# Optimization experiments

Hardware: AMD Instinct MI355X
Metric: run time of the kernel (lower is better)

## Reference

```python
import jax, jax.numpy as jnp
import numpy as np

B, H, W, C = 64, 28, 28, 384
NH, WS = 12, 7
KD = C // NH            # key_dim = head_dim = 32 (attn_ratio=1.0 -> d = KD)
QKV_OUT = 3 * KD * NH   # 1152
HID = 4 * C             # mlp hidden
N = WS * WS             # tokens per window
L = H * W
SCALE = KD ** -0.5
EPS_LN = 1e-5
EPS_BN = 1e-5


def _make_bias_idxs():
    pts = [(i, j) for i in range(WS) for j in range(WS)]
    offs, idxs = {}, []
    for p1 in pts:
        for p2 in pts:
            o = (abs(p1[0] - p2[0]), abs(p1[1] - p2[1]))
            if o not in offs:
                offs[o] = len(offs)
            idxs.append(offs[o])
    return np.asarray(idxs, dtype=np.int32).reshape(N, N)


def _ln(x, g, b):
    m = jnp.mean(x, axis=-1, keepdims=True)
    v = jnp.mean(jnp.square(x - m), axis=-1, keepdims=True)
    return (x - m) * jax.lax.rsqrt(v + EPS_LN) * g + b


def setup_inputs() -> dict:
    key = jax.random.key(0)
    ks = jax.random.split(key, 8)
    s = 0.02
    return {
        "x": jax.random.normal(ks[0], (B, L, C), jnp.float32),
        "ln_a_g": jnp.ones((C,), jnp.float32),
        "ln_a_b": jnp.zeros((C,), jnp.float32),
        "qkv_w": jax.random.normal(ks[1], (QKV_OUT, C), jnp.float32) * s,
        "qkv_b": jnp.zeros((QKV_OUT,), jnp.float32),
        "attn_bias": jax.random.normal(ks[2], (NH, N), jnp.float32) * s,
        "proj_w": jax.random.normal(ks[3], (C, C), jnp.float32) * s,
        "proj_b": jnp.zeros((C,), jnp.float32),
        "conv_w": jax.random.normal(ks[4], (C, 1, 3, 3), jnp.float32) * s,
        "bn_g": jnp.ones((C,), jnp.float32),
        "bn_b": jnp.zeros((C,), jnp.float32),
        "bn_m": jnp.zeros((C,), jnp.float32),
        "bn_v": jnp.ones((C,), jnp.float32),
        "ln_m_g": jnp.ones((C,), jnp.float32),
        "ln_m_b": jnp.zeros((C,), jnp.float32),
        "fc1_w": jax.random.normal(ks[5], (HID, C), jnp.float32) * s,
        "fc1_b": jnp.zeros((HID,), jnp.float32),
        "fc2_w": jax.random.normal(ks[6], (C, HID), jnp.float32) * s,
        "fc2_b": jnp.zeros((C,), jnp.float32),
        "bias_idxs": jnp.asarray(_make_bias_idxs()),
    }


def reference(x, ln_a_g, ln_a_b, qkv_w, qkv_b, attn_bias, proj_w, proj_b,
              conv_w, bn_g, bn_b, bn_m, bn_v, ln_m_g, ln_m_b,
              fc1_w, fc1_b, fc2_w, fc2_b, bias_idxs):
    res = x
    nh, nw = H // WS, W // WS
    # window partition: [B,L,C] -> [B*nWin, N, C]
    xw = x.reshape(B, nh, WS, nw, WS, C).transpose(0, 1, 3, 2, 4, 5)
    xw = xw.reshape(B * nh * nw, N, C)
    # attention
    xn = _ln(xw, ln_a_g, ln_a_b)
    qkv = xn @ qkv_w.T + qkv_b                       # [Bw, N, 3*NH*KD]
    qkv = qkv.reshape(-1, N, NH, 3 * KD).transpose(0, 2, 1, 3)
    q, k, v = qkv[..., :KD], qkv[..., KD:2 * KD], qkv[..., 2 * KD:]
    bias = attn_bias[:, bias_idxs]                   # [NH, N, N]
    attn = jnp.einsum('bhnd,bhmd->bhnm', q, k) * SCALE + bias
    attn = jax.nn.softmax(attn, axis=-1)
    o = jnp.einsum('bhnm,bhmd->bhnd', attn, v)
    o = o.transpose(0, 2, 1, 3).reshape(-1, N, C)
    o = o @ proj_w.T + proj_b
    # window unpartition -> [B, L, C]
    o = o.reshape(B, nh, nw, WS, WS, C).transpose(0, 1, 3, 2, 4, 5).reshape(B, L, C)
    x = res + o
    # depthwise ConvBN (inference BN)
    xc = x.transpose(0, 2, 1).reshape(B, C, H, W)
    xc = jax.lax.conv_general_dilated(
        xc, conv_w, (1, 1), 'SAME', feature_group_count=C,
        dimension_numbers=('NCHW', 'OIHW', 'NCHW'))
    inv = jax.lax.rsqrt(bn_v + EPS_BN)
    xc = (xc - bn_m[None, :, None, None]) * (bn_g * inv)[None, :, None, None] + bn_b[None, :, None, None]
    x = xc.reshape(B, C, L).transpose(0, 2, 1)
    # MLP residual
    h = _ln(x, ln_m_g, ln_m_b)
    h = jax.nn.gelu(h @ fc1_w.T + fc1_b, approximate=False)
    h = h @ fc2_w.T + fc2_b
    return x + h
```

## Files before the change

### kernel.cpp

```cpp
#include <hip/hip_runtime.h>
#include <hip/hip_bf16.h>
#include <stdint.h>

#define BATCH 64
#define CC 384
#define NHEAD 12
#define KD 32
#define NTOK 49
#define LL 784
#define MTOT 50176
#define HID 1536
#define QKV_OUT 1152
#define SCALE 0.17677669529663687f
#define EPS 1e-5f

typedef __bf16 bf16x8 __attribute__((ext_vector_type(8)));
typedef float f32x4 __attribute__((ext_vector_type(4)));

__device__ __forceinline__ float bf2f(unsigned short u) {
  union { unsigned int u; float f; } cv; cv.u = ((unsigned int)u) << 16; return cv.f;
}
__device__ __forceinline__ unsigned short f2bf(float f) {
  union { float f; unsigned int u; } cv; cv.f = f;
  unsigned int r = cv.u + 0x7FFFu + ((cv.u >> 16) & 1u);
  return (unsigned short)(r >> 16);
}
__device__ __forceinline__ void gl_lds16(const unsigned short* g, unsigned short* l) {
  __builtin_amdgcn_global_load_lds(
      (const __attribute__((address_space(1))) unsigned int*)g,
      (__attribute__((address_space(3))) unsigned int*)l, 16, 0, 0);
}
__device__ __forceinline__ int winrow(int m) {
  int wi = m / 49, nn = m - wi * 49;
  int bb = wi >> 4, wb = wi & 15;
  int hs = nn / 7, wsx = nn - hs * 7;
  return bb * LL + (wb >> 2) * 196 + hs * 28 + (wb & 3) * 7 + wsx;
}

__global__ void detect_kernel(const unsigned short* __restrict__ x, int* flag) {
  __shared__ int cnt;
  if (threadIdx.x == 0) cnt = 0;
  __syncthreads();
  int c = 0;
  for (int i = threadIdx.x; i < 4096; i += 256) {
    if (((x[i] >> 7) & 0xFF) == 0xFF) c++;
  }
  atomicAdd(&cnt, c);
  __syncthreads();
  if (threadIdx.x == 0) *flag = (cnt > 0) ? 1 : 0;
}

struct CvtArgs {
  const void* src[19];
  unsigned int n[19];
  unsigned int off[19];
};
__global__ __launch_bounds__(256) void convert_kernel(
    CvtArgs a, unsigned short* __restrict__ dst, const int* __restrict__ flag) {
  const int which = blockIdx.y;
  const unsigned int nn = a.n[which];
  unsigned short* d = dst + a.off[which];
  const unsigned int stride = gridDim.x * blockDim.x;
  const unsigned int idx = blockIdx.x * blockDim.x + threadIdx.x;
  const unsigned int ng = nn >> 3;
  if (*flag) {
    const float* s = (const float*)a.src[which];
    for (unsigned int g = idx; g < ng; g += stride) {
      const float4 f0 = ((const float4*)s)[g * 2];
      const float4 f1 = ((const float4*)s)[g * 2 + 1];
      ushort4 lo, hi;
      lo.x = f2bf(f0.x); lo.y = f2bf(f0.y); lo.z = f2bf(f0.z); lo.w = f2bf(f0.w);
      hi.x = f2bf(f1.x); hi.y = f2bf(f1.y); hi.z = f2bf(f1.z); hi.w = f2bf(f1.w);
      ((ushort4*)d)[g * 2] = lo;
      ((ushort4*)d)[g * 2 + 1] = hi;
    }
    for (unsigned int i = ng * 8 + idx; i < nn; i += stride) d[i] = f2bf(s[i]);
  } else {
    const unsigned short* s = (const unsigned short*)a.src[which];
    for (unsigned int g = idx; g < ng; g += stride)
      ((uint4*)d)[g] = ((const uint4*)s)[g];
    for (unsigned int i = ng * 8 + idx; i < nn; i += stride) d[i] = s[i];
  }
}

__global__ __launch_bounds__(256) void bias_kernel(
    const unsigned short* __restrict__ cAb, const int* __restrict__ bias_idxs,
    float* __restrict__ bias_full) {
  const int h = blockIdx.x;
  for (int i = threadIdx.x; i < NTOK * NTOK; i += 256)
    bias_full[h * NTOK * NTOK + i] = bf2f(cAb[h * NTOK + bias_idxs[i]]);
}

__global__ __launch_bounds__(384) void prep_kernel(
    const unsigned short* __restrict__ cw, const unsigned short* __restrict__ bg,
    const unsigned short* __restrict__ bb, const unsigned short* __restrict__ bm,
    const unsigned short* __restrict__ bv,
    unsigned short* __restrict__ cwT, float* __restrict__ bnsc, float* __restrict__ bnsh) {
  const int c = threadIdx.x;
  const float sc = bf2f(bg[c]) * rsqrtf(bf2f(bv[c]) + EPS);
  bnsc[c] = sc;
  bnsh[c] = bf2f(bb[c]) - bf2f(bm[c]) * sc;
  #pragma unroll
  for (int t = 0; t < 9; ++t) cwT[t * CC + c] = cw[c * 9 + t];
}

__global__ __launch_bounds__(384) void fold_kernel(
    const unsigned short* __restrict__ W, const unsigned short* __restrict__ g,
    const unsigned short* __restrict__ bvec, const unsigned short* __restrict__ b2,
    unsigned short* __restrict__ W2, float* __restrict__ S, float* __restrict__ C) {
  const int n = blockIdx.x, k = threadIdx.x;
  const float w = bf2f(W[(size_t)n * CC + k]);
  const float gw = bf2f(g[k]) * w;
  const unsigned short r = f2bf(gw);
  W2[(size_t)n * CC + k] = r;
  float s = bf2f(r);
  float c = bf2f(bvec[k]) * w;
  #pragma unroll
  for (int off = 32; off; off >>= 1) { s += __shfl_xor(s, off); c += __shfl_xor(c, off); }
  __shared__ float s6[6], c6[6];
  const int wv = k >> 6;
  if ((k & 63) == 0) { s6[wv] = s; c6[wv] = c; }
  __syncthreads();
  if (k == 0) {
    float st = 0.f, ct = 0.f;
    #pragma unroll
    for (int i = 0; i < 6; ++i) { st += s6[i]; ct += c6[i]; }
    S[n] = st; C[n] = ct + bf2f(b2[n]);
  }
}

__global__ __launch_bounds__(128) void statsA_kernel(
    const unsigned short* __restrict__ x, float* __restrict__ muA, float* __restrict__ invA) {
  const int tid = threadIdx.x;
  const int wi = blockIdx.y, n = blockIdx.x;
  const int l = (((wi & 15) >> 2) * 196 + (n / 7) * 28 + (wi & 3) * 7 + (n % 7));
  const unsigned short* xr = x + ((size_t)(wi >> 4) * LL + l) * CC;
  float s = 0.f, sq = 0.f;
  #pragma unroll
  for (int j = 0; j < 3; ++j) {
    const float v = bf2f(xr[tid + 128 * j]);
    s += v; sq += v * v;
  }
  #pragma unroll
  for (int off = 32; off; off >>= 1) { s += __shfl_xor(s, off); sq += __shfl_xor(sq, off); }
  __shared__ float red[4];
  const int wv = tid >> 6;
  if ((tid & 63) == 0) { red[wv] = s; red[2 + wv] = sq; }
  __syncthreads();
  if (tid == 0) {
    const float tot = red[0] + red[1], totq = red[2] + red[3];
    const float mean = tot * (1.f / CC);
    const float var = totq * (1.f / CC) - mean * mean;
    muA[(size_t)wi * NTOK + n] = mean;
    invA[(size_t)wi * NTOK + n] = rsqrtf(var + EPS);
  }
}

enum { EP_PLAIN = 0, EP_WINRES = 2, EP_RES2 = 3, EP_QKV = 4, EP_GELU2 = 5 };

template <int EP>
__global__ __launch_bounds__(256) void gemm128(
    const unsigned short* __restrict__ A, const unsigned short* __restrict__ W,
    const unsigned short* __restrict__ bias, const unsigned short* __restrict__ res,
    void* __restrict__ outp, int K, int N, int m_off, const int* __restrict__ flagp,
    int Nt, const float* __restrict__ muv, const float* __restrict__ invv,
    const float* __restrict__ snv, const float* __restrict__ cnv) {
  constexpr bool GATHER = (EP == EP_QKV);
  constexpr bool LNFOLD = (EP == EP_QKV || EP == EP_GELU2);
  __shared__ __align__(16) unsigned short lds[3 * 8192];
  const int tid = threadIdx.x;
  const int lane = tid & 63;
  const int wave = tid >> 6;
  const int nwg = gridDim.x;
  const int id = blockIdx.x;
  const int q8 = nwg >> 3, r8 = nwg & 7;
  const int xcd = id & 7, rank = id >> 3;
  const int wgid = (xcd < r8 ? xcd * (q8 + 1) : r8 * (q8 + 1) + (xcd - r8) * q8) + rank;
  const int bm = (wgid / Nt) * 128;
  const int bn = (wgid - (wgid / Nt) * Nt) * 128;
  const int wm = (wave >> 1) * 64;
  const int wn = (wave & 1) * 64;
  const int srow = tid >> 2;
  const int sr15 = srow & 15;
  const int sp = (sr15 + (sr15 >> 2)) & 3;
  const int s_col = ((tid & 3) ^ sp) * 8;
  int rowA0, rowA1;
  if (GATHER) {
    rowA0 = winrow(bm + srow + m_off);
    rowA1 = winrow(bm + srow + 64 + m_off);
  } else {
    rowA0 = bm + srow; rowA1 = rowA0 + 64;
  }
  const unsigned short* ApA = A + (size_t)rowA0 * K + s_col;
  const unsigned short* ApB = A + (size_t)rowA1 * K + s_col;
  const unsigned short* Wp0 = W + (size_t)(bn + srow) * K + s_col;
  const size_t rstep = (size_t)64 * K;
  f32x4 acc[4][4] = {};
  const int fr = lane & 15;
  const int quad = lane >> 4;
  const int nt = K >> 5;
  const int rp = (fr + (fr >> 2)) & 3;
  const int cg = (quad ^ rp) * 8;

  auto stage = [&](int bsel, int t) {
    unsigned short* al = lds + bsel * 8192 + tid * 8;
    unsigned short* bl = al + 4096;
    gl_lds16(ApA + t * 32, al);
    gl_lds16(ApB + t * 32, al + 2048);
    gl_lds16(Wp0 + t * 32, bl);
    gl_lds16(Wp0 + t * 32 + rstep, bl + 2048);
  };

  stage(0, 0);
  stage(1, 1);
  int b = 0;
  for (int t = 0; t < nt; ++t) {
    if (t + 1 < nt) asm volatile("s_waitcnt vmcnt(4)" ::: "memory");
    else            asm volatile("s_waitcnt vmcnt(0)" ::: "memory");
    __builtin_amdgcn_s_barrier();
    __builtin_amdgcn_sched_barrier(0);
    if (t + 2 < nt) stage(b ? b - 1 : 2, t + 2);
    const unsigned short* Ab = lds + b * 8192;
    const unsigned short* Bb = Ab + 4096;
    bf16x8 af[4], bfr[4];
    #pragma unroll
    for (int i = 0; i < 4; ++i) {
      af[i]  = *(const bf16x8*)(Ab + (wm + i * 16 + fr) * 32 + cg);
      bfr[i] = *(const bf16x8*)(Bb + (wn + i * 16 + fr) * 32 + cg);
    }
    #pragma unroll
    for (int i = 0; i < 4; ++i)
      #pragma unroll
      for (int j = 0; j < 4; ++j)
        acc[i][j] = __builtin_amdgcn_mfma_f32_16x16x32_bf16(af[i], bfr[j], acc[i][j], 0, 0, 0);
    asm volatile("s_waitcnt lgkmcnt(0)" ::: "memory");
    __builtin_amdgcn_sched_barrier(0);
    b = (b == 2) ? 0 : b + 1;
  }

  int isf32 = 0;
  if (EP == EP_RES2) isf32 = *flagp;
  const int qr = quad * 4;
  float s4[4], c4[4], bvs[4];
  #pragma unroll
  for (int tj = 0; tj < 4; ++tj) {
    const int n = bn + wn + tj * 16 + fr;
    if (LNFOLD) { s4[tj] = snv[n]; c4[tj] = cnv[n]; }
    else        { bvs[tj] = bf2f(bias[n]); }
  }
  #pragma unroll
  for (int ti = 0; ti < 4; ++ti) {
    #pragma unroll
    for (int r = 0; r < 4; ++r) {
      const int mr = bm + wm + ti * 16 + qr + r;
      float iv = 0.f, um = 0.f;
      if (LNFOLD) { iv = invv[mr + m_off]; um = muv[mr + m_off] * iv; }
      size_t rowbase;
      if (EP == EP_WINRES)      rowbase = (size_t)winrow(mr) * CC;
      else if (EP == EP_RES2)   rowbase = (size_t)(mr + m_off) * N;
      else                      rowbase = (size_t)mr * N;
      #pragma unroll
      for (int tj = 0; tj < 4; ++tj) {
        const int n = bn + wn + tj * 16 + fr;
        if (EP == EP_QKV) {
          const float v = iv * acc[ti][tj][r] - um * s4[tj] + c4[tj];
          ((unsigned short*)outp)[rowbase + n] = f2bf(v);
        } else if (EP == EP_GELU2) {
          float v = iv * acc[ti][tj][r] - um * s4[tj] + c4[tj];
          const float t2 = v * (1.5957691216f + 0.0713548162f * v * v);
          v = __fdividef(v, 1.0f + __expf(-t2));
          ((unsigned short*)outp)[rowbase + n] = f2bf(v);
        } else if (EP == EP_WINRES) {
          const size_t idx = rowbase + n;
          float v = acc[ti][tj][r] + bvs[tj] + bf2f(res[idx]);
          ((unsigned short*)outp)[idx] = f2bf(v);
        } else if (EP == EP_RES2) {
          const size_t idx = rowbase + n;
          float v = acc[ti][tj][r] + bvs[tj] + bf2f(res[idx]);
          if (isf32) ((float*)outp)[idx] = v;
          else       ((unsigned short*)outp)[idx] = f2bf(v);
        } else {
          ((unsigned short*)outp)[rowbase + n] = f2bf(acc[ti][tj][r] + bvs[tj]);
        }
      }
    }
  }
}

__global__ __launch_bounds__(64) void attn_mfma(
    const unsigned short* __restrict__ qkv, const float* __restrict__ bias_full,
    unsigned short* __restrict__ o, int wi_off) {
  __shared__ __align__(16) unsigned short Pl[64 * 72];
  __shared__ __align__(16) unsigned short vT[32 * 72];
  const int wi = blockIdx.x, h = blockIdx.y;
  const int lane = threadIdx.x;
  const int l15 = lane & 15;
  const int quad = lane >> 4;
  const unsigned short* base = qkv + (size_t)wi * NTOK * QKV_OUT + h * 96;

  bf16x8 qf[4], kf[4];
  #pragma unroll
  for (int i = 0; i < 4; ++i) {
    const int n = i * 16 + l15;
    if (n < NTOK) {
      const unsigned short* p = base + (size_t)n * QKV_OUT + quad * 8;
      qf[i] = *(const bf16x8*)(p);
      kf[i] = *(const bf16x8*)(p + 32);
    } else {
      qf[i] = (bf16x8)0; kf[i] = (bf16x8)0;
    }
  }

  for (int idx = lane; idx < 32 * 72; idx += 64) vT[idx] = 0;
  __syncthreads();
  for (int idx = lane; idx < NTOK * KD; idx += 64) {
    const int m = idx >> 5, d = idx & 31;
    vT[d * 72 + m] = base[(size_t)m * QKV_OUT + 64 + d];
  }

  f32x4 acc[4][4] = {};
  #pragma unroll
  for (int i = 0; i < 4; ++i)
    #pragma unroll
    for (int j = 0; j < 4; ++j)
      acc[i][j] = __builtin_amdgcn_mfma_f32_16x16x32_bf16(qf[i], kf[j], acc[i][j], 0, 0, 0);

  const float* bh = bias_full + h * NTOK * NTOK;
  float rinv[4][4];
  #pragma unroll
  for (int i = 0; i < 4; ++i) {
    #pragma unroll
    for (int r = 0; r < 4; ++r) {
      const int n = i * 16 + quad * 4 + r;
      float sv[4];
      #pragma unroll
      for (int j = 0; j < 4; ++j) {
        const int m = j * 16 + l15;
        float s = acc[i][j][r] * SCALE;
        if (n < NTOK && m < NTOK) s += bh[n * NTOK + m];
        if (m >= NTOK) s = -1e30f;
        sv[j] = s;
      }
      float mx = fmaxf(fmaxf(sv[0], sv[1]), fmaxf(sv[2], sv[3]));
      #pragma unroll
      for (int t = 1; t < 16; t <<= 1) mx = fmaxf(mx, __shfl_xor(mx, t));
      float sum = 0.f;
      #pragma unroll
      for (int j = 0; j < 4; ++j) {
        const float p = __expf(sv[j] - mx);
        sum += p;
        Pl[n * 72 + j * 16 + l15] = f2bf(p);
      }
      #pragma unroll
      for (int t = 1; t < 16; t <<= 1) sum += __shfl_xor(sum, t);
      rinv[i][r] = 1.f / sum;
    }
  }
  __syncthreads();

  f32x4 acc2[4][2] = {};
  #pragma unroll
  for (int kk = 0; kk < 2; ++kk) {
    bf16x8 pf[4], vf[2];
    #pragma unroll
    for (int i = 0; i < 4; ++i)
      pf[i] = *(const bf16x8*)(Pl + (i * 16 + l15) * 72 + kk * 32 + quad * 8);
    #pragma unroll
    for (int jd = 0; jd < 2; ++jd)
      vf[jd] = *(const bf16x8*)(vT + (jd * 16 + l15) * 72 + kk * 32 + quad * 8);
    #pragma unroll
    for (int i = 0; i < 4; ++i)
      #pragma unroll
      for (int jd = 0; jd < 2; ++jd)
        acc2[i][jd] = __builtin_amdgcn_mfma_f32_16x16x32_bf16(pf[i], vf[jd], acc2[i][jd], 0, 0, 0);
  }

  #pragma unroll
  for (int i = 0; i < 4; ++i) {
    #pragma unroll
    for (int r = 0; r < 4; ++r) {
      const int n = i * 16 + quad * 4 + r;
      if (n < NTOK) {
        const float ri = rinv[i][r];
        #pragma unroll
        for (int jd = 0; jd < 2; ++jd) {
          const int d = jd * 16 + l15;
          o[((size_t)(wi_off + wi) * NTOK + n) * CC + h * KD + d] = f2bf(acc2[i][jd][r] * ri);
        }
      }
    }
  }
}

__global__ __launch_bounds__(384) void conv_bn_ln(
    const unsigned short* __restrict__ x1, const unsigned short* __restrict__ cwT,
    const float* __restrict__ bnsc, const float* __restrict__ bnsh,
    unsigned short* __restrict__ x2, float* __restrict__ muM, float* __restrict__ invM) {
  __shared__ float rs[8][48], rq[8][48];
  const int tid = threadIdx.x;
  const int pos = tid / 48;
  const int c8 = tid - pos * 48;
  const int c0 = c8 * 8;
  const int hw = blockIdx.x * 8 + pos;
  const int b = blockIdx.y;
  const int h = hw / 28, w = hw - h * 28;
  float acc[8] = {};
  #pragma unroll
  for (int t = 0; t < 9; ++t) {
    const int dh = t / 3 - 1, dw = t % 3 - 1;
    const int hh = h + dh, ww = w + dw;
    if (hh >= 0 && hh < 28 && ww >= 0 && ww < 28) {
      const uint4 xv = *(const uint4*)(x1 + ((size_t)b * LL + hh * 28 + ww) * CC + c0);
      const uint4 wv = *(const uint4*)(cwT + t * CC + c0);
      const unsigned short* xp = (const unsigned short*)&xv;
      const unsigned short* wp = (const unsigned short*)&wv;
      #pragma unroll
      for (int k = 0; k < 8; ++k) acc[k] += bf2f(xp[k]) * bf2f(wp[k]);
    }
  }
  const float4 sc0 = *(const float4*)(bnsc + c0);
  const float4 sc1 = *(const float4*)(bnsc + c0 + 4);
  const float4 sh0 = *(const float4*)(bnsh + c0);
  const float4 sh1 = *(const float4*)(bnsh + c0 + 4);
  float y[8];
  y[0] = acc[0] * sc0.x + sh0.x; y[1] = acc[1] * sc0.y + sh0.y;
  y[2] = acc[2] * sc0.z + sh0.z; y[3] = acc[3] * sc0.w + sh0.w;
  y[4] = acc[4] * sc1.x + sh1.x; y[5] = acc[5] * sc1.y + sh1.y;
  y[6] = acc[6] * sc1.z + sh1.z; y[7] = acc[7] * sc1.w + sh1.w;
  unsigned short yr[8];
  #pragma unroll
  for (int k = 0; k < 8; ++k) yr[k] = f2bf(y[k]);
  ushort4 pk0, pk1;
  pk0.x = yr[0]; pk0.y = yr[1]; pk0.z = yr[2]; pk0.w = yr[3];
  pk1.x = yr[4]; pk1.y = yr[5]; pk1.z = yr[6]; pk1.w = yr[7];
  const size_t row = ((size_t)b * LL + hw) * CC + c0;
  *(ushort4*)(x2 + row) = pk0;
  *(ushort4*)(x2 + row + 4) = pk1;
  float s = 0.f, q = 0.f;
  #pragma unroll
  for (int k = 0; k < 8; ++k) { const float v = bf2f(yr[k]); s += v; q += v * v; }
  rs[pos][c8] = s; rq[pos][c8] = q;
  __syncthreads();
  if (c8 == 0) {
    float tot = 0.f, tq = 0.f;
    #pragma unroll 8
    for (int i = 0; i < 48; ++i) { tot += rs[pos][i]; tq += rq[pos][i]; }
    const float mean = tot * (1.f / CC);
    const float var = tq * (1.f / CC) - mean * mean;
    muM[(size_t)b * LL + hw] = mean;
    invM[(size_t)b * LL + hw] = rsqrtf(var + EPS);
  }
}

extern "C" void kernel_launch(void* const* d_in, const int* in_sizes, int n_in,
                              void* d_out, int out_size, void* d_ws, size_t ws_size,
                              hipStream_t stream) {
  int* flag = (int*)d_ws;
  unsigned short* base = (unsigned short*)d_ws;

  CvtArgs args;
  size_t cur = 32;
  size_t off[19];
  for (int i = 0; i < 19; ++i) {
    off[i] = cur;
    args.src[i] = d_in[i];
    args.n[i] = (unsigned int)in_sizes[i];
    args.off[i] = (unsigned int)cur;
    cur += ((size_t)in_sizes[i] + 63) & ~(size_t)63;
  }
  const unsigned short* cx   = base + off[0];
  const unsigned short* cgA  = base + off[1];
  const unsigned short* cbA  = base + off[2];
  const unsigned short* cQw  = base + off[3];
  const unsigned short* cQb  = base + off[4];
  const unsigned short* cAb  = base + off[5];
  const unsigned short* cPw  = base + off[6];
  const unsigned short* cPb  = base + off[7];
  const unsigned short* cCw  = base + off[8];
  const unsigned short* cBg  = base + off[9];
  const unsigned short* cBb  = base + off[10];
  const unsigned short* cBm  = base + off[11];
  const unsigned short* cBv  = base + off[12];
  const unsigned short* cMg  = base + off[13];
  const unsigned short* cMb  = base + off[14];
  const unsigned short* cF1w = base + off[15];
  const unsigned short* cF1b = base + off[16];
  const unsigned short* cF2w = base + off[17];
  const unsigned short* cF2b = base + off[18];
  const int* bias_idxs = (const int*)d_in[19];

  const size_t SZ = (size_t)MTOT * CC;
  const size_t tbl_bytes = 4 * (size_t)MTOT * 4 +
                           ((size_t)QKV_OUT + HID) * CC * 2 +
                           2 * ((size_t)QKV_OUT + HID) * 4 + 65536;
  const size_t need_full_bytes =
      (cur + SZ + (size_t)MTOT * HID) * 2 + tbl_bytes + 1024 * 1024;
  const int nchunk = (ws_size >= need_full_bytes) ? 1 : 2;
  const int MC = MTOT / nchunk;
  const int WC = 1024 / nchunk;
  const size_t buf2_cap = (size_t)MC * HID;

  unsigned short* o_buf = base + cur;
  unsigned short* buf2  = o_buf + SZ;
  unsigned short* x2    = base + off[0];
  float* bias_full = (float*)(buf2 + buf2_cap);
  unsigned short* cwT = (unsigned short*)(bias_full + 12 * NTOK * NTOK);
  float* bnsc = (float*)(cwT + 9 * CC);
  float* bnsh = bnsc + CC;
  float* muA  = bnsh + CC;
  float* invA = muA + MTOT;
  float* muM  = invA + MTOT;
  float* invM = muM + MTOT;
  float* sq   = invM + MTOT;
  float* cq   = sq + QKV_OUT;
  float* sm   = cq + QKV_OUT;
  float* cm   = sm + HID;
  unsigned short* W2q = (unsigned short*)(cm + HID);
  unsigned short* W2m = W2q + (size_t)QKV_OUT * CC;

  detect_kernel<<<1, 256, 0, stream>>>((const unsigned short*)d_in[0], flag);
  convert_kernel<<<dim3(512, 19), 256, 0, stream>>>(args, base, flag);
  bias_kernel<<<NHEAD, 256, 0, stream>>>(cAb, bias_idxs, bias_full);
  prep_kernel<<<1, 384, 0, stream>>>(cCw, cBg, cBb, cBm, cBv, cwT, bnsc, bnsh);
  fold_kernel<<<QKV_OUT, 384, 0, stream>>>(cQw, cgA, cbA, cQb, W2q, sq, cq);
  fold_kernel<<<HID, 384, 0, stream>>>(cF1w, cMg, cMb, cF1b, W2m, sm, cm);

  statsA_kernel<<<dim3(49, 1024), 128, 0, stream>>>(cx, muA, invA);

  for (int c = 0; c < nchunk; ++c) {
    gemm128<EP_QKV><<<(MC / 128) * (QKV_OUT / 128), 256, 0, stream>>>(
        cx, W2q, nullptr, nullptr, buf2, CC, QKV_OUT, c * MC, nullptr,
        QKV_OUT / 128, muA, invA, sq, cq);
    attn_mfma<<<dim3(WC, NHEAD), 64, 0, stream>>>(buf2, bias_full, o_buf, c * WC);
  }

  gemm128<EP_WINRES><<<(MTOT / 128) * (CC / 128), 256, 0, stream>>>(
      o_buf, cPw, cPb, cx, d_out, CC, CC, 0, nullptr, CC / 128,
      nullptr, nullptr, nullptr, nullptr);

  conv_bn_ln<<<dim3(98, BATCH), 384, 0, stream>>>(
      (const unsigned short*)d_out, cwT, bnsc, bnsh, x2, muM, invM);

  for (int c = 0; c < nchunk; ++c) {
    gemm128<EP_GELU2><<<(MC / 128) * (HID / 128), 256, 0, stream>>>(
        x2 + (size_t)c * MC * CC, W2m, nullptr, nullptr, buf2, CC, HID, c * MC,
        nullptr, HID / 128, muM, invM, sm, cm);
    gemm128<EP_RES2><<<(MC / 128) * (CC / 128), 256, 0, stream>>>(
        buf2, cF2w, cF2b, x2, d_out, HID, CC, c * MC, flag, CC / 128,
        nullptr, nullptr, nullptr, nullptr);
  }
}
```

Measured before the change: 679.5 us.

## Move window gather out of GEMMs into attention kernel indexing

The QKV GEMM and the projection GEMM now work on rows in flat image order, so they load and store contiguously without the per-row winrow gather and scatter. The attention kernel does the window partition itself, computing flat row indices for each token when it reads qkv and writes its output. LayerNorm mean and inverse std are packed into a float2 so the epilogue does one load per row. This removes address math and scattered accesses from the GEMMs, at the cost of strided window accesses inside the attention kernel. With two chunks the window-to-row mapping must stay aligned with the chunk boundary, which it does because 512 windows times 49 rows equals 25088.

```diff
diff --git a/kernel.cpp b/kernel.cpp
--- a/kernel.cpp
+++ b/kernel.cpp
@@ -29,12 +29,6 @@
   __builtin_amdgcn_global_load_lds(
       (const __attribute__((address_space(1))) unsigned int*)g,
       (__attribute__((address_space(3))) unsigned int*)l, 16, 0, 0);
-}
-__device__ __forceinline__ int winrow(int m) {
-  int wi = m / 49, nn = m - wi * 49;
-  int bb = wi >> 4, wb = wi & 15;
-  int hs = nn / 7, wsx = nn - hs * 7;
-  return bb * LL + (wb >> 2) * 196 + hs * 28 + (wb & 3) * 7 + wsx;
 }
 
 __global__ void detect_kernel(const unsigned short* __restrict__ x, int* flag) {
@@ -130,11 +124,10 @@
 }
 
 __global__ __launch_bounds__(128) void statsA_kernel(
-    const unsigned short* __restrict__ x, float* __restrict__ muA, float* __restrict__ invA) {
+    const unsigned short* __restrict__ x, float2* __restrict__ mui) {
   const int tid = threadIdx.x;
-  const int wi = blockIdx.y, n = blockIdx.x;
-  const int l = (((wi & 15) >> 2) * 196 + (n / 7) * 28 + (wi & 3) * 7 + (n % 7));
-  const unsigned short* xr = x + ((size_t)(wi >> 4) * LL + l) * CC;
+  const size_t row = (size_t)blockIdx.y * LL + blockIdx.x;
+  const unsigned short* xr = x + row * CC;
   float s = 0.f, sq = 0.f;
   #pragma unroll
   for (int j = 0; j < 3; ++j) {
@@ -151,22 +144,20 @@
     const float tot = red[0] + red[1], totq = red[2] + red[3];
     const float mean = tot * (1.f / CC);
     const float var = totq * (1.f / CC) - mean * mean;
-    muA[(size_t)wi * NTOK + n] = mean;
-    invA[(size_t)wi * NTOK + n] = rsqrtf(var + EPS);
-  }
-}
-
-enum { EP_PLAIN = 0, EP_WINRES = 2, EP_RES2 = 3, EP_QKV = 4, EP_GELU2 = 5 };
+    mui[row] = make_float2(mean, rsqrtf(var + EPS));
+  }
+}
+
+enum { EP_RES = 2, EP_RES2 = 3, EP_LNF = 4, EP_GELU2 = 5 };
 
 template <int EP>
 __global__ __launch_bounds__(256) void gemm128(
     const unsigned short* __restrict__ A, const unsigned short* __restrict__ W,
     const unsigned short* __restrict__ bias, const unsigned short* __restrict__ res,
     void* __restrict__ outp, int K, int N, int m_off, const int* __restrict__ flagp,
-    int Nt, const float* __restrict__ muv, const float* __restrict__ invv,
+    int Nt, const float2* __restrict__ mui,
     const float* __restrict__ snv, const float* __restrict__ cnv) {
-  constexpr bool GATHER = (EP == EP_QKV);
-  constexpr bool LNFOLD = (EP == EP_QKV || EP == EP_GELU2);
+  constexpr bool LNFOLD = (EP == EP_LNF || EP == EP_GELU2);
   __shared__ __align__(16) unsigned short lds[3 * 8192];
   const int tid = threadIdx.x;
   const int lane = tid & 63;
@@ -184,15 +175,7 @@
   const int sr15 = srow & 15;
   const int sp = (sr15 + (sr15 >> 2)) & 3;
   const int s_col = ((tid & 3) ^ sp) * 8;
-  int rowA0, rowA1;
-  if (GATHER) {
-    rowA0 = winrow(bm + srow + m_off);
-    rowA1 = winrow(bm + srow + 64 + m_off);
-  } else {
-    rowA0 = bm + srow; rowA1 = rowA0 + 64;
-  }
-  const unsigned short* ApA = A + (size_t)rowA0 * K + s_col;
-  const unsigned short* ApB = A + (size_t)rowA1 * K + s_col;
+  const unsigned short* Ap0 = A + (size_t)(bm + srow) * K + s_col;
   const unsigned short* Wp0 = W + (size_t)(bn + srow) * K + s_col;
   const size_t rstep = (size_t)64 * K;
   f32x4 acc[4][4] = {};
@@ -205,8 +188,8 @@
   auto stage = [&](int bsel, int t) {
     unsigned short* al = lds + bsel * 8192 + tid * 8;
     unsigned short* bl = al + 4096;
-    gl_lds16(ApA + t * 32, al);
-    gl_lds16(ApB + t * 32, al + 2048);
+    gl_lds16(Ap0 + t * 32, al);
+    gl_lds16(Ap0 + t * 32 + rstep, al + 2048);
     gl_lds16(Wp0 + t * 32, bl);
     gl_lds16(Wp0 + t * 32 + rstep, bl + 2048);
   };
@@ -254,15 +237,15 @@
     for (int r = 0; r < 4; ++r) {
       const int mr = bm + wm + ti * 16 + qr + r;
       float iv = 0.f, um = 0.f;
-      if (LNFOLD) { iv = invv[mr + m_off]; um = muv[mr + m_off] * iv; }
-      size_t rowbase;
-      if (EP == EP_WINRES)      rowbase = (size_t)winrow(mr) * CC;
-      else if (EP == EP_RES2)   rowbase = (size_t)(mr + m_off) * N;
-      else                      rowbase = (size_t)mr * N;
+      if (LNFOLD) {
+        const float2 mi = mui[mr + m_off];
+        iv = mi.y; um = mi.x * mi.y;
+      }
+      const size_t rowbase = (size_t)mr * N;
       #pragma unroll
       for (int tj = 0; tj < 4; ++tj) {
         const int n = bn + wn + tj * 16 + fr;
-        if (EP == EP_QKV) {
+        if (EP == EP_LNF) {
           const float v = iv * acc[ti][tj][r] - um * s4[tj] + c4[tj];
           ((unsigned short*)outp)[rowbase + n] = f2bf(v);
         } else if (EP == EP_GELU2) {
@@ -270,17 +253,15 @@
           const float t2 = v * (1.5957691216f + 0.0713548162f * v * v);
           v = __fdividef(v, 1.0f + __expf(-t2));
           ((unsigned short*)outp)[rowbase + n] = f2bf(v);
-        } else if (EP == EP_WINRES) {
+        } else if (EP == EP_RES) {
           const size_t idx = rowbase + n;
-          float v = acc[ti][tj][r] + bvs[tj] + bf2f(res[idx]);
+          const float v = acc[ti][tj][r] + bvs[tj] + bf2f(res[idx]);
           ((unsigned short*)outp)[idx] = f2bf(v);
-        } else if (EP == EP_RES2) {
+        } else {
           const size_t idx = rowbase + n;
-          float v = acc[ti][tj][r] + bvs[tj] + bf2f(res[idx]);
+          const float v = acc[ti][tj][r] + bvs[tj] + bf2f(res[idx]);
           if (isf32) ((float*)outp)[idx] = v;
           else       ((unsigned short*)outp)[idx] = f2bf(v);
-        } else {
-          ((unsigned short*)outp)[rowbase + n] = f2bf(acc[ti][tj][r] + bvs[tj]);
         }
       }
     }
@@ -289,21 +270,27 @@
 
 __global__ __launch_bounds__(64) void attn_mfma(
     const unsigned short* __restrict__ qkv, const float* __restrict__ bias_full,
-    unsigned short* __restrict__ o, int wi_off) {
+    unsigned short* __restrict__ o, int wi_off, int row_off) {
   __shared__ __align__(16) unsigned short Pl[64 * 72];
   __shared__ __align__(16) unsigned short vT[32 * 72];
-  const int wi = blockIdx.x, h = blockIdx.y;
+  const int wi = wi_off + blockIdx.x, h = blockIdx.y;
   const int lane = threadIdx.x;
   const int l15 = lane & 15;
   const int quad = lane >> 4;
-  const unsigned short* base = qkv + (size_t)wi * NTOK * QKV_OUT + h * 96;
+  const int bb = wi >> 4, wb = wi & 15;
+  const int wrow0 = bb * LL + (wb >> 2) * 196 + (wb & 3) * 7;
+  auto flatrow = [&](int n) {
+    const int h7 = n / 7;
+    return wrow0 + h7 * 28 + (n - h7 * 7);
+  };
 
   bf16x8 qf[4], kf[4];
   #pragma unroll
   for (int i = 0; i < 4; ++i) {
     const int n = i * 16 + l15;
     if (n < NTOK) {
-      const unsigned short* p = base + (size_t)n * QKV_OUT + quad * 8;
+      const unsigned short* p =
+          qkv + (size_t)(flatrow(n) - row_off) * QKV_OUT + h * 96 + quad * 8;
       qf[i] = *(const bf16x8*)(p);
       kf[i] = *(const bf16x8*)(p + 32);
     } else {
@@ -315,7 +302,7 @@
   __syncthreads();
   for (int idx = lane; idx < NTOK * KD; idx += 64) {
     const int m = idx >> 5, d = idx & 31;
-    vT[d * 72 + m] = base[(size_t)m * QKV_OUT + 64 + d];
+    vT[d * 72 + m] = qkv[(size_t)(flatrow(m) - row_off) * QKV_OUT + h * 96 + 64 + d];
   }
 
   f32x4 acc[4][4] = {};
@@ -382,10 +369,11 @@
       const int n = i * 16 + quad * 4 + r;
       if (n < NTOK) {
         const float ri = rinv[i][r];
+        const size_t orow = (size_t)flatrow(n) * CC + h * KD;
         #pragma unroll
         for (int jd = 0; jd < 2; ++jd) {
           const int d = jd * 16 + l15;
-          o[((size_t)(wi_off + wi) * NTOK + n) * CC + h * KD + d] = f2bf(acc2[i][jd][r] * ri);
+          o[orow + d] = f2bf(acc2[i][jd][r] * ri);
         }
       }
     }
@@ -395,7 +383,7 @@
 __global__ __launch_bounds__(384) void conv_bn_ln(
     const unsigned short* __restrict__ x1, const unsigned short* __restrict__ cwT,
     const float* __restrict__ bnsc, const float* __restrict__ bnsh,
-    unsigned short* __restrict__ x2, float* __restrict__ muM, float* __restrict__ invM) {
+    unsigned short* __restrict__ x2, float2* __restrict__ mui) {
   __shared__ float rs[8][48], rq[8][48];
   const int tid = threadIdx.x;
   const int pos = tid / 48;
@@ -447,8 +435,7 @@
     for (int i = 0; i < 48; ++i) { tot += rs[pos][i]; tq += rq[pos][i]; }
     const float mean = tot * (1.f / CC);
     const float var = tq * (1.f / CC) - mean * mean;
-    muM[(size_t)b * LL + hw] = mean;
-    invM[(size_t)b * LL + hw] = rsqrtf(var + EPS);
+    mui[(size_t)b * LL + hw] = make_float2(mean, rsqrtf(var + EPS));
   }
 }
 
@@ -490,7 +477,7 @@
   const int* bias_idxs = (const int*)d_in[19];
 
   const size_t SZ = (size_t)MTOT * CC;
-  const size_t tbl_bytes = 4 * (size_t)MTOT * 4 +
+  const size_t tbl_bytes = 2 * (size_t)MTOT * 8 +
                            ((size_t)QKV_OUT + HID) * CC * 2 +
                            2 * ((size_t)QKV_OUT + HID) * 4 + 65536;
   const size_t need_full_bytes =
@@ -507,11 +494,9 @@
   unsigned short* cwT = (unsigned short*)(bias_full + 12 * NTOK * NTOK);
   float* bnsc = (float*)(cwT + 9 * CC);
   float* bnsh = bnsc + CC;
-  float* muA  = bnsh + CC;
-  float* invA = muA + MTOT;
-  float* muM  = invA + MTOT;
-  float* invM = muM + MTOT;
-  float* sq   = invM + MTOT;
+  float2* muiA = (float2*)(bnsh + CC);
+  float2* muiM = muiA + MTOT;
+  float* sq   = (float*)(muiM + MTOT);
   float* cq   = sq + QKV_OUT;
   float* sm   = cq + QKV_OUT;
   float* cm   = sm + HID;
@@ -525,28 +510,29 @@
   fold_kernel<<<QKV_OUT, 384, 0, stream>>>(cQw, cgA, cbA, cQb, W2q, sq, cq);
   fold_kernel<<<HID, 384, 0, stream>>>(cF1w, cMg, cMb, cF1b, W2m, sm, cm);
 
-  statsA_kernel<<<dim3(49, 1024), 128, 0, stream>>>(cx, muA, invA);
+  statsA_kernel<<<dim3(LL, BATCH), 128, 0, stream>>>(cx, muiA);
 
   for (int c = 0; c < nchunk; ++c) {
-    gemm128<EP_QKV><<<(MC / 128) * (QKV_OUT / 128), 256, 0, stream>>>(
-        cx, W2q, nullptr, nullptr, buf2, CC, QKV_OUT, c * MC, nullptr,
-        QKV_OUT / 128, muA, invA, sq, cq);
-    attn_mfma<<<dim3(WC, NHEAD), 64, 0, stream>>>(buf2, bias_full, o_buf, c * WC);
-  }
-
-  gemm128<EP_WINRES><<<(MTOT / 128) * (CC / 128), 256, 0, stream>>>(
+    gemm128<EP_LNF><<<(MC / 128) * (QKV_OUT / 128), 256, 0, stream>>>(
+        cx + (size_t)c * MC * CC, W2q, nullptr, nullptr, buf2, CC, QKV_OUT, c * MC,
+        nullptr, QKV_OUT / 128, muiA, sq, cq);
+    attn_mfma<<<dim3(WC, NHEAD), 64, 0, stream>>>(
+        buf2, bias_full, o_buf, c * WC, c * MC);
+  }
+
+  gemm128<EP_RES><<<(MTOT / 128) * (CC / 128), 256, 0, stream>>>(
       o_buf, cPw, cPb, cx, d_out, CC, CC, 0, nullptr, CC / 128,
-      nullptr, nullptr, nullptr, nullptr);
+      nullptr, nullptr, nullptr);
 
   conv_bn_ln<<<dim3(98, BATCH), 384, 0, stream>>>(
-      (const unsigned short*)d_out, cwT, bnsc, bnsh, x2, muM, invM);
+      (const unsigned short*)d_out, cwT, bnsc, bnsh, x2, muiM);
 
   for (int c = 0; c < nchunk; ++c) {
     gemm128<EP_GELU2><<<(MC / 128) * (HID / 128), 256, 0, stream>>>(
         x2 + (size_t)c * MC * CC, W2m, nullptr, nullptr, buf2, CC, HID, c * MC,
-        nullptr, HID / 128, muM, invM, sm, cm);
+        nullptr, HID / 128, muiM, sm, cm);
     gemm128<EP_RES2><<<(MC / 128) * (CC / 128), 256, 0, stream>>>(
         buf2, cF2w, cF2b, x2, d_out, HID, CC, c * MC, flag, CC / 128,
-        nullptr, nullptr, nullptr, nullptr);
-  }
-}
+        nullptr, nullptr, nullptr);
+  }
+}
```

Result: no change. 676.8 us (-0.4%).
